# Performance work log

Hardware: AMD Instinct MI355X
Metric: run time of the kernel (lower is better)

## Reference

```python
import jax, jax.numpy as jnp
import numpy as np

DIM = 1024
N_HEADS = 16
HEAD_DIM = DIM // N_HEADS
MAX_CTX = 2048


def build_rope_cache(seq_len, head_dim, base=10000.0):
    inv_freq = 1.0 / (base ** (jnp.arange(0, head_dim, 2, dtype=jnp.float32) / head_dim))
    t = jnp.arange(seq_len, dtype=jnp.float32)
    freqs = jnp.einsum('i,j->ij', t, inv_freq)  # [T, head_dim//2]
    return jnp.cos(freqs), jnp.sin(freqs)


def apply_rope(x, cos, sin):
    # x: [B, H, T, D]; interleaved even/odd rotation
    x1 = x[..., 0::2]
    x2 = x[..., 1::2]
    c = cos[None, None, :x.shape[-2], :]
    s = sin[None, None, :x.shape[-2], :]
    rx1 = x1 * c - x2 * s
    rx2 = x1 * s + x2 * c
    return jnp.stack([rx1, rx2], axis=-1).reshape(x.shape)


def setup_inputs() -> dict:
    key = jax.random.key(0)
    k1, k2, k3 = jax.random.split(key, 3)
    B, T = 2, 2048
    x = jax.random.normal(k1, (B, T, DIM), dtype=jnp.float32)
    # torch nn.Linear weight shapes: [out_features, in_features]
    qkv_w = jax.random.normal(k2, (3 * DIM, DIM), dtype=jnp.float32) * (1.0 / np.sqrt(DIM))
    out_w = jax.random.normal(k3, (DIM, DIM), dtype=jnp.float32) * (1.0 / np.sqrt(DIM))
    return {"x": x, "qkv_w": qkv_w, "out_w": out_w}


def reference(x, qkv_w, out_w):
    B, T, C = x.shape
    cos, sin = build_rope_cache(MAX_CTX, HEAD_DIM)
    cos = cos.astype(x.dtype)
    sin = sin.astype(x.dtype)

    qkv = jnp.einsum('btc,dc->btd', x, qkv_w)  # [B, T, 3C]
    qkv = qkv.reshape(B, T, 3, N_HEADS, HEAD_DIM).transpose(2, 0, 3, 1, 4)
    q, k, v = qkv[0], qkv[1], qkv[2]  # each [B, H, T, D]

    q = apply_rope(q, cos, sin)
    k = apply_rope(k, cos, sin)

    scale = 1.0 / np.sqrt(HEAD_DIM)
    scores = jnp.einsum('bhqd,bhkd->bhqk', q, k) * scale  # [B, H, T, T]
    causal = jnp.tril(jnp.ones((T, T), dtype=bool))
    scores = jnp.where(causal[None, None], scores, jnp.finfo(scores.dtype).min)
    attn = jax.nn.softmax(scores, axis=-1)
    y = jnp.einsum('bhqk,bhkd->bhqd', attn, v)  # [B, H, T, D]
    y = y.transpose(0, 2, 1, 3).reshape(B, T, C)
    return jnp.einsum('btc,dc->btd', y, out_w)
```

## Files before the change

### kernel.cpp

```cpp
#include <hip/hip_runtime.h>
#include <hip/hip_bf16.h>
#include <cstdint>
#include <cstddef>

#define B_SZ   2
#define T_CTX  2048
#define DIM_C  1024
#define NHEAD  16
#define HD     64
#define NBH    (B_SZ*NHEAD)

typedef __attribute__((ext_vector_type(8))) short short8;
typedef __attribute__((ext_vector_type(4))) float f32x4;
typedef __attribute__((ext_vector_type(16))) float f32x16;

union BV8 { short8 s; __hip_bfloat16 h[8]; unsigned short u[8]; };
union U32x4 { uint32_t u[4]; short8 s8; };

#define GLD16(gp, lp) \
  __builtin_amdgcn_global_load_lds((const __attribute__((address_space(1))) void*)(gp), \
                                   (__attribute__((address_space(3))) void*)(lp), 16, 0, 0)

__device__ inline uint32_t pkbf(float a, float b) {
  union { __hip_bfloat16 h; unsigned short u; } ua, ub;
  ua.h = __float2bfloat16(a);
  ub.h = __float2bfloat16(b);
  return ((uint32_t)ub.u << 16) | (uint32_t)ua.u;
}

__global__ __launch_bounds__(256) void cvt_all(const float* __restrict__ x,
                                               const float* __restrict__ wq,
                                               const float* __restrict__ wo,
                                               __hip_bfloat16* __restrict__ xb,
                                               __hip_bfloat16* __restrict__ wqb,
                                               __hip_bfloat16* __restrict__ wob) {
  int i = blockIdx.x * 256 + threadIdx.x;
  const float* src;
  __hip_bfloat16* dst;
  int off;
  if (i < 1048576) { src = x; dst = xb; off = i; }
  else if (i < 1835008) { src = wq; dst = wqb; off = i - 1048576; }
  else { src = wo; dst = wob; off = i - 1835008; }
  float4 v = reinterpret_cast<const float4*>(src)[off];
  BV8 o;
  o.h[0] = __float2bfloat16(v.x);
  o.h[1] = __float2bfloat16(v.y);
  o.h[2] = __float2bfloat16(v.z);
  o.h[3] = __float2bfloat16(v.w);
  ushort4 st = { o.u[0], o.u[1], o.u[2], o.u[3] };
  reinterpret_cast<ushort4*>(dst)[off] = st;
}

template <typename OutT, int BN>
__global__ __launch_bounds__(256) void gemm_bt(const __hip_bfloat16* __restrict__ A,
                                               const __hip_bfloat16* __restrict__ Bt,
                                               OutT* __restrict__ C,
                                               int M, int N, int K) {
  constexpr int NB = BN / 32;
  constexpr int ABYT = 128 * 128;
  constexpr int BBYT = BN * 128;
  __shared__ __align__(16) char smem[2 * (ABYT + BBYT)];
  const int tid = threadIdx.x;
  const int w = tid >> 6, l = tid & 63;
  const int l15 = l & 15, l4 = l >> 4;
  const int wr = w >> 1, wc = w & 1;
  const int gx = (int)gridDim.x;
  const int nwg = gx * (int)gridDim.y;
  int lin = (int)blockIdx.y * gx + (int)blockIdx.x;
  lin = (lin & 7) * (nwg >> 3) + (lin >> 3);
  const long bm = (long)(lin / gx) * 128;
  const long bn = (long)(lin % gx) * BN;

  f32x4 acc[4][NB] = {};

  const int srow = tid >> 3;
  const int scol = (tid & 7) * 16;
  const int ssw  = scol ^ ((srow & 7) << 4);
  const char* Ab  = (const char*)A;
  const char* Btb = (const char*)Bt;

#define GSTAGE(kt_, buf_)                                                                \
  {                                                                                      \
    char* base_ = smem + (buf_) * (ABYT + BBYT);                                         \
    _Pragma("unroll")                                                                    \
    for (int it = 0; it < 4; ++it) {                                                     \
      long arow = bm + it * 32 + srow;                                                   \
      GLD16(Ab + (arow * K + (kt_)) * 2 + ssw, base_ + it * 4096 + w * 1024);            \
    }                                                                                    \
    _Pragma("unroll")                                                                    \
    for (int it = 0; it < BN / 32; ++it) {                                               \
      long brow = bn + it * 32 + srow;                                                   \
      GLD16(Btb + (brow * K + (kt_)) * 2 + ssw, base_ + ABYT + it * 4096 + w * 1024);    \
    }                                                                                    \
  }

  GSTAGE(0, 0)

  int cur = 0;
  for (int kt = 0; kt < K; kt += 64) {
    __syncthreads();
    if (kt + 64 < K) GSTAGE(kt + 64, cur ^ 1)
    const char* Ac = smem + cur * (ABYT + BBYT);
    const char* Bc = Ac + ABYT;
#pragma unroll
    for (int ksub = 0; ksub < 2; ++ksub) {
      short8 aF[4], bF[NB];
#pragma unroll
      for (int m = 0; m < 4; ++m) {
        int R = wr * 64 + m * 16 + l15;
        aF[m] = *(const short8*)(Ac + R * 128 + ((ksub * 64 + l4 * 16) ^ ((R & 7) << 4)));
      }
#pragma unroll
      for (int n = 0; n < NB; ++n) {
        int R = wc * (BN / 2) + n * 16 + l15;
        bF[n] = *(const short8*)(Bc + R * 128 + ((ksub * 64 + l4 * 16) ^ ((R & 7) << 4)));
      }
#pragma unroll
      for (int m = 0; m < 4; ++m)
#pragma unroll
        for (int n = 0; n < NB; ++n)
          acc[m][n] = __builtin_amdgcn_mfma_f32_16x16x32_bf16(aF[m], bF[n], acc[m][n], 0, 0, 0);
    }
    cur ^= 1;
  }
#undef GSTAGE

#pragma unroll
  for (int m = 0; m < 4; ++m)
#pragma unroll
    for (int n = 0; n < NB; ++n)
#pragma unroll
      for (int r = 0; r < 4; ++r) {
        long row = bm + wr * 64 + m * 16 + l4 * 4 + r;
        long col = bn + wc * (BN / 2) + n * 16 + l15;
        float v = acc[m][n][r];
        if constexpr (sizeof(OutT) == 2) {
          C[row * N + col] = __float2bfloat16(v);
        } else {
          C[row * N + col] = v;
        }
      }
}

__global__ __launch_bounds__(256) void rope_pack(const __hip_bfloat16* __restrict__ qkv,
                                                 __hip_bfloat16* __restrict__ Qb,
                                                 __hip_bfloat16* __restrict__ Kb,
                                                 __hip_bfloat16* __restrict__ VTb) {
  __shared__ __hip_bfloat16 vt[64][72];
  const int bh = blockIdx.x;
  const int b = bh >> 4, h = bh & 15;
  const int t0 = blockIdx.y * 64;
  const int tid = threadIdx.x;
  const float QSCL = 0.125f * 1.4426950408889634f;

#pragma unroll
  for (int rep = 0; rep < 2; ++rep) {
    int idx = rep * 256 + tid;
    int tt = idx >> 3;
    int d0 = (idx & 7) * 8;
    int t = t0 + tt;
    size_t src = ((size_t)(b * T_CTX + t)) * 3072 + h * 64 + d0;
    BV8 qv, kv, vv, qo, ko;
    qv.s = *(const short8*)(qkv + src);
    kv.s = *(const short8*)(qkv + src + 1024);
    vv.s = *(const short8*)(qkv + src + 2048);
#pragma unroll
    for (int p = 0; p < 4; ++p) {
      int i = (d0 >> 1) + p;
      float inv = exp2f(-13.287712379549449f * ((float)(2 * i) * (1.0f / 64.0f)));
      float ang = (float)t * inv;
      float sn, cn;
      sincosf(ang, &sn, &cn);
      float q1 = __bfloat162float(qv.h[2 * p]);
      float q2 = __bfloat162float(qv.h[2 * p + 1]);
      float k1 = __bfloat162float(kv.h[2 * p]);
      float k2 = __bfloat162float(kv.h[2 * p + 1]);
      qo.h[2 * p]     = __float2bfloat16((q1 * cn - q2 * sn) * QSCL);
      qo.h[2 * p + 1] = __float2bfloat16((q1 * sn + q2 * cn) * QSCL);
      ko.h[2 * p]     = __float2bfloat16(k1 * cn - k2 * sn);
      ko.h[2 * p + 1] = __float2bfloat16(k1 * sn + k2 * cn);
    }
    size_t dst = ((size_t)bh * T_CTX + t) * 64 + d0;
    *(short8*)(Qb + dst) = qo.s;
    *(short8*)(Kb + dst) = ko.s;
#pragma unroll
    for (int j = 0; j < 8; ++j) vt[d0 + j][tt] = vv.h[j];
  }
  __syncthreads();
#pragma unroll
  for (int rep = 0; rep < 2; ++rep) {
    int idx = rep * 256 + tid;
    int d = idx >> 3;
    int toff = (idx & 7) * 8;
    BV8 o;
#pragma unroll
    for (int j = 0; j < 8; ++j) o.h[j] = vt[d][toff + j];
    *(short8*)(VTb + ((size_t)bh * 64 + d) * T_CTX + t0 + toff) = o.s;
  }
}

__global__ __launch_bounds__(256) void flash_attn(const __hip_bfloat16* __restrict__ Qb,
                                                  const __hip_bfloat16* __restrict__ Kb,
                                                  const __hip_bfloat16* __restrict__ VTb,
                                                  __hip_bfloat16* __restrict__ Y) {
  __shared__ __align__(16) char smem[65536];
  const int bh = blockIdx.x;
  const int b = bh >> 4, h = bh & 15;
  const int y = blockIdx.y;
  const int jA = 31 - y;
  const int jB = y;
  const int tid = threadIdx.x;
  const int w = tid >> 6, l = tid & 63;
  const int qsub = w >> 1, kh = w & 1;
  const int l31 = l & 31, hh = l >> 5;
  const int sw7 = (l31 & 7) << 4;
  const int rowb = tid >> 3;
  const int colS = (tid & 7) * 16;

#define STAGE1(gg)                                                                     \
  {                                                                                    \
    const int tt_ = ((gg) <= jA) ? (gg) : (gg) - jA - 1;                               \
    const int kv0_ = tt_ << 6;                                                         \
    char* base_ = smem + (((gg) >> 1) & 1) * 32768 + ((gg) & 1) * 16384;               \
    _Pragma("unroll")                                                                  \
    for (int rnd = 0; rnd < 2; ++rnd) {                                                \
      int row = rnd * 32 + rowb;                                                       \
      int sw = colS ^ ((row & 7) << 4);                                                \
      GLD16((const char*)Kb + (((size_t)bh * T_CTX + kv0_ + row) << 7) + sw,           \
            base_ + rnd * 4096 + w * 1024);                                            \
      GLD16((const char*)VTb + ((((size_t)bh * 64 + row) * T_CTX + kv0_) << 1) + sw,   \
            base_ + 8192 + rnd * 4096 + w * 1024);                                     \
    }                                                                                  \
  }

  f32x16 oA0 = {}, oA1 = {}, oB0 = {}, oB1 = {};
  float lrA = 0.0f, lrB = 0.0f;

  STAGE1(0)
  STAGE1(1)

  int rr = 0;
#pragma unroll
  for (int ph = 0; ph < 2; ++ph) {
    const int j = ph ? jB : jA;
    const int qglob = j * 64 + qsub * 32 + l31;
    f32x16& od0 = ph ? oB0 : oA0;
    f32x16& od1 = ph ? oB1 : oA1;
    float& lrw = ph ? lrB : lrA;

    short8 qB[4];
#pragma unroll
    for (int dblk = 0; dblk < 4; ++dblk)
      qB[dblk] = *(const short8*)(Qb + ((size_t)bh * T_CTX + qglob) * 64 + dblk * 16 + hh * 8);

    for (int t = 0; t <= j; ++t, ++rr) {
      if ((rr & 1) == 0) {
        __syncthreads();
        if (rr + 2 <= 32) STAGE1(rr + 2)
        if (rr + 3 <= 32) STAGE1(rr + 3)
      }
      const char* KsB = smem + ((rr >> 1) & 1) * 32768 + (rr & 1) * 16384;
      const char* VsB = KsB + 8192;
      const int kv0 = t << 6;
      const bool lastT = (t == j);

      if (!(lastT && kh > qsub)) {
        short8 kA[4];
#pragma unroll
        for (int dblk = 0; dblk < 4; ++dblk)
          kA[dblk] = *(const short8*)(KsB + (kh * 32 + l31) * 128 + ((dblk * 32 + hh * 16) ^ sw7));
        short8 vA[2][2];
#pragma unroll
        for (int dt = 0; dt < 2; ++dt)
#pragma unroll
          for (int ks = 0; ks < 2; ++ks)
            vA[dt][ks] = *(const short8*)(VsB + (dt * 32 + l31) * 128 +
                                          ((kh * 64 + ks * 32 + hh * 16) ^ sw7));

        f32x16 sT = {};
#pragma unroll
        for (int dblk = 0; dblk < 4; ++dblk) {
          __builtin_amdgcn_s_setprio(1);
          sT = __builtin_amdgcn_mfma_f32_32x32x16_bf16(kA[dblk], qB[dblk], sT, 0, 0, 0);
          __builtin_amdgcn_s_setprio(0);
        }
        if (lastT && kh == qsub) {
          const int kbase = kv0 + kh * 32 + 4 * hh;
#pragma unroll
          for (int r = 0; r < 16; ++r) {
            int kg = kbase + (r & 3) + 8 * (r >> 2);
            sT[r] = (kg > qglob) ? -1e30f : sT[r];
          }
        }
        float s8[8];
#pragma unroll
        for (int i = 0; i < 8; ++i) {
          sT[i]     = __builtin_amdgcn_exp2f(sT[i]);
          sT[i + 8] = __builtin_amdgcn_exp2f(sT[i + 8]);
          s8[i] = sT[i] + sT[i + 8];
        }
        lrw += ((s8[0] + s8[1]) + (s8[2] + s8[3])) + ((s8[4] + s8[5]) + (s8[6] + s8[7]));
        uint32_t wk[8];
#pragma unroll
        for (int i = 0; i < 8; ++i) wk[i] = pkbf(sT[2 * i], sT[2 * i + 1]);
#pragma unroll
        for (int ks = 0; ks < 2; ++ks) {
          const int base = ks * 4;
          uint32_t own0 = wk[base + 0], own1 = wk[base + 1];
          uint32_t own2 = wk[base + 2], own3 = wk[base + 3];
          uint32_t e0 = (uint32_t)__shfl_xor((int)(hh ? own0 : own2), 32);
          uint32_t e1 = (uint32_t)__shfl_xor((int)(hh ? own1 : own3), 32);
          U32x4 u;
          u.u[0] = hh ? e0 : own0;
          u.u[1] = hh ? e1 : own1;
          u.u[2] = hh ? own2 : e0;
          u.u[3] = hh ? own3 : e1;
          __builtin_amdgcn_s_setprio(1);
          od0 = __builtin_amdgcn_mfma_f32_32x32x16_bf16(vA[0][ks], u.s8, od0, 0, 0, 0);
          od1 = __builtin_amdgcn_mfma_f32_32x32x16_bf16(vA[1][ks], u.s8, od1, 0, 0, 0);
          __builtin_amdgcn_s_setprio(0);
        }
      }
    }
  }

  lrA += __shfl_xor(lrA, 32);
  lrB += __shfl_xor(lrB, 32);

  __syncthreads();
  {
    float* exch = (float*)smem;
    float* lst = exch + 8192;
    const int slotA = (0 * 2 + qsub) * 2 + kh;
    const int slotB = (1 * 2 + qsub) * 2 + kh;
    const f32x16& nA = kh ? oA0 : oA1;
    const f32x16& nB = kh ? oB0 : oB1;
#pragma unroll
    for (int m = 0; m < 4; ++m) {
      int c = ((2 * m + hh) ^ (l31 & 7)) * 4;
      f32x4 va, vb;
#pragma unroll
      for (int i = 0; i < 4; ++i) { va[i] = nA[m * 4 + i]; vb[i] = nB[m * 4 + i]; }
      *(f32x4*)(exch + slotA * 1024 + l31 * 32 + c) = va;
      *(f32x4*)(exch + slotB * 1024 + l31 * 32 + c) = vb;
    }
    if (hh == 0) {
      lst[slotA * 32 + l31] = lrA;
      lst[slotB * 32 + l31] = lrB;
    }
    __syncthreads();
    const int pA = (0 * 2 + qsub) * 2 + (kh ^ 1);
    const int pB = (1 * 2 + qsub) * 2 + (kh ^ 1);
    float ltA = lrA + lst[pA * 32 + l31];
    float ltB = lrB + lst[pB * 32 + l31];
    f32x16& ownA = kh ? oA1 : oA0;
    f32x16& ownB = kh ? oB1 : oB0;
#pragma unroll
    for (int m = 0; m < 4; ++m) {
      int c = ((2 * m + hh) ^ (l31 & 7)) * 4;
      f32x4 aA = *(const f32x4*)(exch + pA * 1024 + l31 * 32 + c);
      f32x4 aB = *(const f32x4*)(exch + pB * 1024 + l31 * 32 + c);
#pragma unroll
      for (int i = 0; i < 4; ++i) { ownA[m * 4 + i] += aA[i]; ownB[m * 4 + i] += aB[i]; }
    }
#pragma unroll
    for (int sl = 0; sl < 2; ++sl) {
      const f32x16& ov = sl ? ownB : ownA;
      float inv = 1.0f / (sl ? ltB : ltA);
      int q0s = (sl ? jB : jA) * 64 + qsub * 32;
      size_t rowoff = ((size_t)(b * T_CTX + q0s + l31)) * DIM_C + h * 64 + kh * 32;
#pragma unroll
      for (int m = 0; m < 4; ++m) {
        union { ushort4 v; unsigned short us[4]; } st;
#pragma unroll
        for (int i = 0; i < 4; ++i) {
          union { __hip_bfloat16 h2; unsigned short u; } cv;
          cv.h2 = __float2bfloat16(ov[m * 4 + i] * inv);
          st.us[i] = cv.u;
        }
        *(ushort4*)(Y + rowoff + 8 * m + 4 * hh) = st.v;
      }
    }
  }
#undef STAGE1
}

extern "C" void kernel_launch(void* const* d_in, const int* in_sizes, int n_in,
                              void* d_out, int out_size, void* d_ws, size_t ws_size,
                              hipStream_t stream) {
  const float* x     = (const float*)d_in[0];
  const float* qkv_w = (const float*)d_in[1];
  const float* out_w = (const float*)d_in[2];
  float* out = (float*)d_out;

  char* ws = (char*)d_ws;
  const size_t MB = 1024 * 1024;
  __hip_bfloat16* xb    = (__hip_bfloat16*)(ws + 0 * MB);
  __hip_bfloat16* wqkvb = (__hip_bfloat16*)(ws + 8 * MB);
  __hip_bfloat16* woutb = (__hip_bfloat16*)(ws + 14 * MB);
  __hip_bfloat16* qkvb  = (__hip_bfloat16*)(ws + 16 * MB);
  __hip_bfloat16* Qb    = (__hip_bfloat16*)(ws + 40 * MB);
  __hip_bfloat16* Kb    = (__hip_bfloat16*)(ws + 48 * MB);
  __hip_bfloat16* VTb   = (__hip_bfloat16*)(ws + 56 * MB);
  __hip_bfloat16* yb    = (__hip_bfloat16*)(ws + 64 * MB);

  cvt_all<<<8192, 256, 0, stream>>>(x, qkv_w, out_w, xb, wqkvb, woutb);

  gemm_bt<__hip_bfloat16, 192><<<dim3(16, 32), 256, 0, stream>>>(xb, wqkvb, qkvb, 4096, 3072, 1024);

  rope_pack<<<dim3(32, 32), 256, 0, stream>>>(qkvb, Qb, Kb, VTb);

  flash_attn<<<dim3(NBH, 16), 256, 0, stream>>>(Qb, Kb, VTb, yb);

  gemm_bt<float, 64><<<dim3(16, 32), 256, 0, stream>>>(yb, woutb, out, 4096, 1024, 1024);
}
```

Baseline: 101.0 us.

## Double flash-attention query tile to 128 rows with 512-thread blocks

Each attention block now covers a 128-row query slab per phase using 8 waves instead of 64 rows with 4 waves, so each staged K/V tile is reused by twice as many query rows. Grid y halves and the block size doubles. The causal mask and skip logic are generalized to per-wave key-range checks, and the LDS exchange area grows for the extra waves. The tradeoff is fewer, larger blocks, which lowers the count of independent workgroups and may reduce occupancy per CU.

```diff
diff --git a/kernel.cpp b/kernel.cpp
--- a/kernel.cpp
+++ b/kernel.cpp
@@ -199,38 +199,36 @@
   }
 }
 
-__global__ __launch_bounds__(256) void flash_attn(const __hip_bfloat16* __restrict__ Qb,
+__global__ __launch_bounds__(512) void flash_attn(const __hip_bfloat16* __restrict__ Qb,
                                                   const __hip_bfloat16* __restrict__ Kb,
                                                   const __hip_bfloat16* __restrict__ VTb,
                                                   __hip_bfloat16* __restrict__ Y) {
-  __shared__ __align__(16) char smem[65536];
+  __shared__ __align__(16) char smem[67584];
   const int bh = blockIdx.x;
   const int b = bh >> 4, h = bh & 15;
   const int y = blockIdx.y;
-  const int jA = 31 - y;
+  const int jA = 15 - y;
   const int jB = y;
+  const int tmaxA = 2 * jA + 1;
+  const int tmaxB = 2 * jB + 1;
   const int tid = threadIdx.x;
   const int w = tid >> 6, l = tid & 63;
   const int qsub = w >> 1, kh = w & 1;
   const int l31 = l & 31, hh = l >> 5;
   const int sw7 = (l31 & 7) << 4;
-  const int rowb = tid >> 3;
-  const int colS = (tid & 7) * 16;
+  const int rowb = w * 8 + (l >> 3);
+  const int colS = (l & 7) * 16;
 
 #define STAGE1(gg)                                                                     \
   {                                                                                    \
-    const int tt_ = ((gg) <= jA) ? (gg) : (gg) - jA - 1;                               \
+    const int tt_ = ((gg) <= tmaxA) ? (gg) : (gg) - tmaxA - 1;                         \
     const int kv0_ = tt_ << 6;                                                         \
     char* base_ = smem + (((gg) >> 1) & 1) * 32768 + ((gg) & 1) * 16384;               \
-    _Pragma("unroll")                                                                  \
-    for (int rnd = 0; rnd < 2; ++rnd) {                                                \
-      int row = rnd * 32 + rowb;                                                       \
-      int sw = colS ^ ((row & 7) << 4);                                                \
-      GLD16((const char*)Kb + (((size_t)bh * T_CTX + kv0_ + row) << 7) + sw,           \
-            base_ + rnd * 4096 + w * 1024);                                            \
-      GLD16((const char*)VTb + ((((size_t)bh * 64 + row) * T_CTX + kv0_) << 1) + sw,   \
-            base_ + 8192 + rnd * 4096 + w * 1024);                                     \
-    }                                                                                  \
+    int sw = colS ^ ((rowb & 7) << 4);                                                 \
+    GLD16((const char*)Kb + (((size_t)bh * T_CTX + kv0_ + rowb) << 7) + sw,            \
+          base_ + w * 1024);                                                           \
+    GLD16((const char*)VTb + ((((size_t)bh * 64 + rowb) * T_CTX + kv0_) << 1) + sw,    \
+          base_ + 8192 + w * 1024);                                                    \
   }
 
   f32x16 oA0 = {}, oA1 = {}, oB0 = {}, oB1 = {};
@@ -242,8 +240,10 @@
   int rr = 0;
 #pragma unroll
   for (int ph = 0; ph < 2; ++ph) {
-    const int j = ph ? jB : jA;
-    const int qglob = j * 64 + qsub * 32 + l31;
+    const int slab = ph ? jB : jA;
+    const int tmax = ph ? tmaxB : tmaxA;
+    const int Q0 = slab * 128 + qsub * 32;
+    const int qglob = Q0 + l31;
     f32x16& od0 = ph ? oB0 : oA0;
     f32x16& od1 = ph ? oB1 : oA1;
     float& lrw = ph ? lrB : lrA;
@@ -253,18 +253,18 @@
     for (int dblk = 0; dblk < 4; ++dblk)
       qB[dblk] = *(const short8*)(Qb + ((size_t)bh * T_CTX + qglob) * 64 + dblk * 16 + hh * 8);
 
-    for (int t = 0; t <= j; ++t, ++rr) {
+    for (int t = 0; t <= tmax; ++t, ++rr) {
       if ((rr & 1) == 0) {
         __syncthreads();
-        if (rr + 2 <= 32) STAGE1(rr + 2)
-        if (rr + 3 <= 32) STAGE1(rr + 3)
+        if (rr + 2 <= 33) STAGE1(rr + 2)
+        if (rr + 3 <= 33) STAGE1(rr + 3)
       }
       const char* KsB = smem + ((rr >> 1) & 1) * 32768 + (rr & 1) * 16384;
       const char* VsB = KsB + 8192;
       const int kv0 = t << 6;
-      const bool lastT = (t == j);
-
-      if (!(lastT && kh > qsub)) {
+      const int kbase0 = kv0 + kh * 32;
+
+      if (kbase0 <= Q0 + 31) {
         short8 kA[4];
 #pragma unroll
         for (int dblk = 0; dblk < 4; ++dblk)
@@ -284,8 +284,8 @@
           sT = __builtin_amdgcn_mfma_f32_32x32x16_bf16(kA[dblk], qB[dblk], sT, 0, 0, 0);
           __builtin_amdgcn_s_setprio(0);
         }
-        if (lastT && kh == qsub) {
-          const int kbase = kv0 + kh * 32 + 4 * hh;
+        if (kbase0 + 31 > Q0) {
+          const int kbase = kbase0 + 4 * hh;
 #pragma unroll
           for (int r = 0; r < 16; ++r) {
             int kg = kbase + (r & 3) + 8 * (r >> 2);
@@ -330,9 +330,9 @@
   __syncthreads();
   {
     float* exch = (float*)smem;
-    float* lst = exch + 8192;
-    const int slotA = (0 * 2 + qsub) * 2 + kh;
-    const int slotB = (1 * 2 + qsub) * 2 + kh;
+    float* lst = exch + 16384;
+    const int slotA = (0 * 4 + qsub) * 2 + kh;
+    const int slotB = (1 * 4 + qsub) * 2 + kh;
     const f32x16& nA = kh ? oA0 : oA1;
     const f32x16& nB = kh ? oB0 : oB1;
 #pragma unroll
@@ -349,8 +349,8 @@
       lst[slotB * 32 + l31] = lrB;
     }
     __syncthreads();
-    const int pA = (0 * 2 + qsub) * 2 + (kh ^ 1);
-    const int pB = (1 * 2 + qsub) * 2 + (kh ^ 1);
+    const int pA = (0 * 4 + qsub) * 2 + (kh ^ 1);
+    const int pB = (1 * 4 + qsub) * 2 + (kh ^ 1);
     float ltA = lrA + lst[pA * 32 + l31];
     float ltB = lrB + lst[pB * 32 + l31];
     f32x16& ownA = kh ? oA1 : oA0;
@@ -367,7 +367,7 @@
     for (int sl = 0; sl < 2; ++sl) {
       const f32x16& ov = sl ? ownB : ownA;
       float inv = 1.0f / (sl ? ltB : ltA);
-      int q0s = (sl ? jB : jA) * 64 + qsub * 32;
+      int q0s = (sl ? jB : jA) * 128 + qsub * 32;
       size_t rowoff = ((size_t)(b * T_CTX + q0s + l31)) * DIM_C + h * 64 + kh * 32;
 #pragma unroll
       for (int m = 0; m < 4; ++m) {
@@ -410,7 +410,7 @@
 
   rope_pack<<<dim3(32, 32), 256, 0, stream>>>(qkvb, Qb, Kb, VTb);
 
-  flash_attn<<<dim3(NBH, 16), 256, 0, stream>>>(Qb, Kb, VTb, yb);
+  flash_attn<<<dim3(NBH, 8), 512, 0, stream>>>(Qb, Kb, VTb, yb);
 
   gemm_bt<float, 64><<<dim3(16, 32), 256, 0, stream>>>(yb, woutb, out, 4096, 1024, 1024);
 }
```

Result: faster. 96.48 us, median of 2 (-4.5%).
